# Performance work log

Measured on AMD Instinct MI355X. Metric: run time of the kernel, lower is better.

Reference implementation:

```python
import jax, jax.numpy as jnp
import numpy as np

HEADS = 8
DIM = 64      # dim
DH = 64       # dim_head
DK = 24       # dim_k (== dim_head_k * heads, required by reshape in forward)
DHK = 3       # dim_head_k (also conv groups)


def setup_inputs() -> dict:
    key = jax.random.key(0)
    ks = jax.random.split(key, 10)
    b, h, w = 4, 128, 128
    return {
        "x_in": jax.random.normal(ks[0], (b, h, w, DIM), jnp.float32),
        "illu_fea_trans": jax.random.normal(ks[1], (b, h, w, DIM), jnp.float32),
        "illu_map_trans": jax.random.normal(ks[2], (b, h, w, DK), jnp.float32),
        # Linear weights stored as [in, out] (torch stores [out, in]; math y = x @ W_in_out)
        "Wq": jax.random.normal(ks[3], (DIM, HEADS * DH), jnp.float32) * 0.05,
        "Wk": jax.random.normal(ks[4], (DK, HEADS * DHK), jnp.float32) * 0.05,
        "Wv": jax.random.normal(ks[5], (DIM, HEADS * DH), jnp.float32) * 0.05,
        "rescale": jnp.ones((HEADS, 1, 1), jnp.float32),
        "Wp": jax.random.normal(ks[6], (HEADS * DHK, DK), jnp.float32) * 0.05,
        "bp": jax.random.normal(ks[7], (DK,), jnp.float32) * 0.05,
        # grouped conv weights, OIHW: [out=24, in/groups=8, 3, 3]
        "conv1_w": jax.random.normal(ks[8], (DK, DK // DHK, 3, 3), jnp.float32) * 0.05,
        "conv2_w": jax.random.normal(ks[9], (DK, DK // DHK, 3, 3), jnp.float32) * 0.05,
    }


def _gconv(x_nchw, w_oihw):
    return jax.lax.conv_general_dilated(
        x_nchw, w_oihw, window_strides=(1, 1), padding='SAME',
        feature_group_count=DHK,
        dimension_numbers=('NCHW', 'OIHW', 'NCHW'))


def reference(x_in, illu_fea_trans, illu_map_trans, Wq, Wk, Wv, rescale, Wp, bp, conv1_w, conv2_w):
    b, h, w, c = x_in.shape
    n = h * w
    # projections
    q = (x_in.reshape(b, n, c) @ Wq).reshape(b, n, HEADS, DH)
    k_inp = illu_map_trans.reshape(b, n, DK) @ Wk            # [b, n, heads*dhk]
    v = (illu_fea_trans.reshape(b, n, c) @ Wv).reshape(b, n, HEADS, DH)
    kh = k_inp.reshape(b, n, HEADS, DHK)
    q = q / (DIM ** 0.5)  # note: scaled by sqrt(dim), not sqrt(dim_head)
    # channel-wise cross-attention: attn over channel dims, contracting tokens n
    attn = jnp.einsum('bnhk,bnhd->bhkd', kh, q) * rescale[None]  # [b, heads, dhk, dh]
    attn = jax.nn.softmax(attn, axis=-1)
    out = jnp.einsum('bhkd,bnhd->bnkh', attn, v)             # [b, n, dhk, heads]
    out = out.reshape(b, n, DHK * HEADS) @ Wp + bp           # proj
    out = out.reshape(b, h, w, DK)
    # positional branch: two grouped 3x3 convs with exact GELU on k_inp
    kx = k_inp.reshape(b, h, w, DK).transpose(0, 3, 1, 2)    # NCHW
    y = _gconv(kx, conv1_w)
    y = jax.nn.gelu(y, approximate=False)
    y = _gconv(y, conv2_w)
    return out + y.transpose(0, 2, 3, 1)
```

## Files before the change

### kernel.cpp

```cpp
#include <hip/hip_runtime.h>
#include <math.h>

#define HEADS 8
#define DIM   64
#define DK    24
#define DHK   3
#define BB    4
#define HH    128
#define WW    128
#define NN    (HH*WW)
#define QSCALE 0.125f

__global__ __launch_bounds__(256) void s_reduce(
    const float* __restrict__ imap,
    const float* __restrict__ x,
    float* __restrict__ Sp_part)
{
    __shared__ __align__(16) float smem[6160];
    float* xs   = smem;
    float* ms   = smem + 4096;
    float* part = smem;

    const int tid = threadIdx.x;
    const int blk = blockIdx.x;
    const int b = blk >> 8, chunk = blk & 255;
    const int w = tid >> 6, lane = tid & 63;
    const int cq = lane & 15;
    const int ig = lane >> 4;

    const long tok0 = (long)b * NN + chunk * 64;

    {
        const float4* xg = (const float4*)(x + tok0 * 64);
        float4* xs4 = (float4*)xs;
        #pragma unroll
        for (int e = 0; e < 4; ++e) xs4[tid + e * 256] = xg[tid + e * 256];
        const float4* mg = (const float4*)(imap + tok0 * 24);
        float4* ms4 = (float4*)ms;
        if (tid < 128) {
            ms4[tid]       = mg[tid];
            ms4[tid + 128] = mg[tid + 128];
            ms4[tid + 256] = mg[tid + 256];
        }
    }
    __syncthreads();

    float acc[6][4];
    #pragma unroll
    for (int r = 0; r < 6; ++r)
        #pragma unroll
        for (int q = 0; q < 4; ++q) acc[r][q] = 0.f;

    {
        const float* xp = xs + w * 16 * 64 + cq * 4;
        const float* mp = ms + w * 16 * 24 + ig * 6;
        #pragma unroll 4
        for (int t = 0; t < 16; ++t) {
            float4 xv = *(const float4*)(xp + t * 64);
            float2 m0 = *(const float2*)(mp + t * 24);
            float2 m1 = *(const float2*)(mp + t * 24 + 2);
            float2 m2 = *(const float2*)(mp + t * 24 + 4);
            float mm[6] = {m0.x, m0.y, m1.x, m1.y, m2.x, m2.y};
            #pragma unroll
            for (int r = 0; r < 6; ++r) {
                acc[r][0] += mm[r] * xv.x;
                acc[r][1] += mm[r] * xv.y;
                acc[r][2] += mm[r] * xv.z;
                acc[r][3] += mm[r] * xv.w;
            }
        }
    }
    __syncthreads();

    float* pp = part + w * 1540;
    #pragma unroll
    for (int r = 0; r < 6; ++r) {
        float4 v = {acc[r][0], acc[r][1], acc[r][2], acc[r][3]};
        *(float4*)(pp + (ig * 6 + r) * 64 + cq * 4) = v;
    }
    __syncthreads();

    for (int e = tid; e < 1536; e += 256) {
        Sp_part[(long)blk * 1536 + e] =
            part[e] + part[1540 + e] + part[3080 + e] + part[4620 + e];
    }
}

__global__ __launch_bounds__(256) void slab_reduce(
    const float* __restrict__ Sp_part,
    float* __restrict__ Sp)
{
    __shared__ float red[256];
    const int tid = threadIdx.x;
    const int blk = blockIdx.x;
    const int b = blk / 24, eg = blk % 24;
    const int w = tid >> 6, lane = tid & 63;
    const int e = eg * 64 + lane;

    const float* p = Sp_part + ((long)(b * 256 + w * 64)) * 1536 + e;
    float s = 0.f;
    #pragma unroll 16
    for (int sb = 0; sb < 64; ++sb) s += p[(long)sb * 1536];
    red[w * 64 + lane] = s;
    __syncthreads();

    if (tid < 64)
        Sp[b * 1536 + eg * 64 + tid] =
            red[tid] + red[64 + tid] + red[128 + tid] + red[192 + tid];
}

__global__ __launch_bounds__(1024) void attn_fused(
    const float* __restrict__ Sp,
    const float* __restrict__ Wk,
    const float* __restrict__ Wq,
    const float* __restrict__ Wv,
    const float* __restrict__ rescale,
    const float* __restrict__ Wp,
    float* __restrict__ Pt)
{
    __shared__ float Sp_l[1536];
    __shared__ float S_l[1536];
    __shared__ float att[1536];

    const int tid = threadIdx.x, b = blockIdx.x;
    const int w = tid >> 6, lane = tid & 63;

    for (int e = tid; e < 1536; e += 1024) Sp_l[e] = Sp[b * 1536 + e];
    __syncthreads();

    for (int e = tid; e < 1536; e += 1024) {
        const int c = e & 63, ch = e >> 6;
        float s = 0.f;
        #pragma unroll
        for (int i = 0; i < 24; ++i) s += Wk[i * 24 + ch] * Sp_l[i * 64 + c];
        S_l[e] = s;
    }
    __syncthreads();

    for (int e = tid; e < 1536; e += 1024) {
        const int d = e & 63, ch = e >> 6, h = ch / 3;
        const float* wq = Wq + h * 64 + d;
        const float* sr = S_l + ch * 64;
        float s = 0.f;
        #pragma unroll 8
        for (int c = 0; c < 64; ++c) s += sr[c] * wq[c * 512];
        att[e] = s * QSCALE * rescale[h];
    }
    __syncthreads();

    #pragma unroll
    for (int pass = 0; pass < 2; ++pass) {
        const int r = w + pass * 16;
        if (r < 24 && (pass == 0 || w < 8)) {
            float a = att[r * 64 + lane];
            float mx = a;
            #pragma unroll
            for (int off = 32; off >= 1; off >>= 1)
                mx = fmaxf(mx, __shfl_xor(mx, off, 64));
            float e = expf(a - mx);
            float sum = e;
            #pragma unroll
            for (int off = 32; off >= 1; off >>= 1)
                sum += __shfl_xor(sum, off, 64);
            att[r * 64 + lane] = e / sum;
        }
    }
    __syncthreads();

    for (int e = tid; e < 1536; e += 1024) {
        const int c = e & 63, ch = e >> 6, h = ch / 3;
        const float* pr = att + ch * 64;
        const float* wv = Wv + c * 512 + h * 64;
        float s = 0.f;
        #pragma unroll
        for (int d = 0; d < 64; ++d) s += pr[d] * wv[d];
        S_l[e] = s;
    }
    __syncthreads();

    for (int e = tid; e < 1536; e += 1024) {
        const int c = e & 63, o = e >> 6;
        float s = 0.f;
        #pragma unroll
        for (int k = 0; k < 3; ++k)
            #pragma unroll
            for (int h = 0; h < 8; ++h)
                s += S_l[(h * 3 + k) * 64 + c] * Wp[(k * 8 + h) * 24 + o];
        Pt[b * 1536 + e] = s;
    }
}

__global__ __launch_bounds__(192, 2) void conv_fused(
    const float* __restrict__ imap, const float* __restrict__ Wk,
    const float* __restrict__ c1w,  const float* __restrict__ fea,
    const float* __restrict__ c2w,  const float* __restrict__ Pt,
    const float* __restrict__ bp,   float* __restrict__ outp)
{
    __shared__ __align__(16) float smem[7152];
    float* kbuf = smem;
    float* feat = smem;
    float* y1l  = smem + 4352;

    const int tid = threadIdx.x;
    const int blk = blockIdx.x;
    const int b = blk >> 8, ti = (blk >> 4) & 15, tj = blk & 15;
    const int i0 = ti * 8, j0 = tj * 8;
    const int o = tid % 24, jj = tid / 24;
    const int g = o >> 3;

    if (tid < 144) {
        const int pi = tid / 12, pj = tid % 12;
        const int gi = i0 + pi - 2, gj = j0 + pj - 2;
        float kv[24];
        #pragma unroll
        for (int j = 0; j < 24; ++j) kv[j] = 0.f;
        if (gi >= 0 && gi < HH && gj >= 0 && gj < WW) {
            const float4* m4 = (const float4*)(imap + (((long)b * HH + gi) * WW + gj) * 24);
            float m[24];
            #pragma unroll
            for (int i = 0; i < 6; ++i) {
                float4 v = m4[i];
                m[4*i+0]=v.x; m[4*i+1]=v.y; m[4*i+2]=v.z; m[4*i+3]=v.w;
            }
            for (int i = 0; i < 24; ++i) {
                float mi = m[i];
                #pragma unroll
                for (int j = 0; j < 24; ++j) kv[j] += mi * Wk[i * 24 + j];
            }
        }
        #pragma unroll
        for (int j = 0; j < 24; ++j) kbuf[tid * 28 + j] = kv[j];
    }
    __syncthreads();

    {
        float wr[8][9];
        {
            const float4* wp = (const float4*)(c1w + o * 72);
            #pragma unroll
            for (int t = 0; t < 18; ++t) ((float4*)wr)[t] = wp[t];
        }
        for (int task = tid; task < 240; task += 192) {
            const int r = task / 24;
            float wc[3][3][8];
            #pragma unroll
            for (int slot = 0; slot < 2; ++slot)
                #pragma unroll
                for (int di = 0; di < 3; ++di) {
                    const float* p = kbuf + ((r + di) * 12 + slot) * 28 + g * 8;
                    *(float4*)&wc[slot][di][0] = *(const float4*)(p);
                    *(float4*)&wc[slot][di][4] = *(const float4*)(p + 4);
                }
            #pragma unroll
            for (int c = 0; c < 10; ++c) {
                const int s2 = (c + 2) % 3;
                #pragma unroll
                for (int di = 0; di < 3; ++di) {
                    const float* p = kbuf + ((r + di) * 12 + (c + 2)) * 28 + g * 8;
                    *(float4*)&wc[s2][di][0] = *(const float4*)(p);
                    *(float4*)&wc[s2][di][4] = *(const float4*)(p + 4);
                }
                float s = 0.f;
                #pragma unroll
                for (int dj = 0; dj < 3; ++dj) {
                    const int sl = (c + dj) % 3;
                    #pragma unroll
                    for (int di = 0; di < 3; ++di)
                        #pragma unroll
                        for (int ic = 0; ic < 8; ++ic)
                            s += wc[sl][di][ic] * wr[ic][di * 3 + dj];
                }
                const int gi = i0 + r - 1, gj = j0 + c - 1;
                float val = 0.f;
                if (gi >= 0 && gi < HH && gj >= 0 && gj < WW)
                    val = 0.5f * s * (1.f + erff(s * 0.70710678f));
                y1l[(r * 10 + c) * 28 + o] = val;
            }
        }
    }
    __syncthreads();

    {
        const float4* feaT4 = (const float4*)(fea + (((long)(b * HH + i0)) * WW + j0) * 64);
        float4* feat4 = (float4*)feat;
        for (int e = tid; e < 1024; e += 192) {
            const int pix = e >> 4, cq = e & 15;
            feat4[pix * 17 + cq] =
                feaT4[((long)(pix >> 3) * WW + (pix & 7)) * 16 + cq];
        }
    }
    __syncthreads();

    float wr[8][9];
    {
        const float4* wp = (const float4*)(c2w + o * 72);
        #pragma unroll
        for (int t = 0; t < 18; ++t) ((float4*)wr)[t] = wp[t];
    }

    float acc[8];
    {
        const float bo = bp[o];
        #pragma unroll
        for (int ii = 0; ii < 8; ++ii) acc[ii] = bo;
        const float4* pr4 = (const float4*)(Pt + b * 1536 + o * 64);
        for (int cq = 0; cq < 16; ++cq) {
            float4 p = pr4[cq];
            #pragma unroll
            for (int ii = 0; ii < 8; ++ii) {
                float4 f = ((const float4*)(feat + (ii * 8 + jj) * 68))[cq];
                acc[ii] += f.x * p.x + f.y * p.y + f.z * p.z + f.w * p.w;
            }
        }
    }

    float win[3][3][8];
    #define LROW(R, SLOT)                                                     \
    {                                                                         \
        const float* rp_ = y1l + ((R) * 10 + jj) * 28 + g * 8;                \
        *(float4*)&win[SLOT][0][0] = *(const float4*)(rp_);                   \
        *(float4*)&win[SLOT][0][4] = *(const float4*)(rp_ + 4);               \
        *(float4*)&win[SLOT][1][0] = *(const float4*)(rp_ + 28);              \
        *(float4*)&win[SLOT][1][4] = *(const float4*)(rp_ + 32);              \
        *(float4*)&win[SLOT][2][0] = *(const float4*)(rp_ + 56);              \
        *(float4*)&win[SLOT][2][4] = *(const float4*)(rp_ + 60);              \
    }

    LROW(0, 0)
    LROW(1, 1)
    #pragma unroll
    for (int ii = 0; ii < 8; ++ii) {
        LROW(ii + 2, (ii + 2) % 3)
        float s = 0.f;
        #pragma unroll
        for (int di = 0; di < 3; ++di) {
            const int slot = (ii + di) % 3;
            #pragma unroll
            for (int dj = 0; dj < 3; ++dj)
                #pragma unroll
                for (int ic = 0; ic < 8; ++ic)
                    s += win[slot][dj][ic] * wr[ic][di * 3 + dj];
        }
        outp[((long)((b * HH + i0 + ii) * WW + j0)) * 24 + tid] = acc[ii] + s;
    }
    #undef LROW
}

extern "C" void kernel_launch(void* const* d_in, const int* in_sizes, int n_in,
                              void* d_out, int out_size, void* d_ws, size_t ws_size,
                              hipStream_t stream) {
    const float* x_in    = (const float*)d_in[0];
    const float* fea     = (const float*)d_in[1];
    const float* imap    = (const float*)d_in[2];
    const float* Wq      = (const float*)d_in[3];
    const float* Wk      = (const float*)d_in[4];
    const float* Wv      = (const float*)d_in[5];
    const float* rescale = (const float*)d_in[6];
    const float* Wp      = (const float*)d_in[7];
    const float* bp      = (const float*)d_in[8];
    const float* c1w     = (const float*)d_in[9];
    const float* c2w     = (const float*)d_in[10];
    float* out = (float*)d_out;

    float* ws      = (float*)d_ws;
    float* Sp_part = ws;
    float* Sp      = ws + 1572864;
    float* Pt      = ws + 1579008;

    s_reduce<<<1024, 256, 0, stream>>>(imap, x_in, Sp_part);
    slab_reduce<<<96, 256, 0, stream>>>(Sp_part, Sp);
    attn_fused<<<4, 1024, 0, stream>>>(Sp, Wk, Wq, Wv, rescale, Wp, Pt);
    conv_fused<<<BB * 256, 192, 0, stream>>>(imap, Wk, c1w, fea, c2w, Pt, bp, out);
}
```

Before: 166.4 us.

## Fold attention projections into reduction kernels and drop the single-block attention kernel

Removes the attn_fused kernel, which ran on only 4 blocks. The Wk and Wq projections move into each s_reduce block, using linearity to project the per-chunk partial sums before the global reduction. The second reduction kernel now also does the softmax and Wv product per row. The Wp projection is recomputed per tile inside conv_fused. This removes one launch and a serialized low-parallelism stage, at the cost of redundant Wq and Wp matmuls in every block, plus extra shared memory and global reads of weights.

```diff
diff --git a/kernel.cpp b/kernel.cpp
--- a/kernel.cpp
+++ b/kernel.cpp
@@ -11,15 +11,21 @@
 #define NN    (HH*WW)
 #define QSCALE 0.125f
 
-__global__ __launch_bounds__(256) void s_reduce(
+__global__ __launch_bounds__(256) void s_reduce_proj(
     const float* __restrict__ imap,
     const float* __restrict__ x,
-    float* __restrict__ Sp_part)
+    const float* __restrict__ Wk,
+    const float* __restrict__ Wq,
+    const float* __restrict__ rescale,
+    float* __restrict__ att_part)
 {
-    __shared__ __align__(16) float smem[6160];
+    __shared__ __align__(16) float smem[7696];
     float* xs   = smem;
     float* ms   = smem + 4096;
     float* part = smem;
+    float* Sp_l = smem + 6160;
+    float* S_l  = smem;
+    float* wq_l = smem + 1536;
 
     const int tid = threadIdx.x;
     const int blk = blockIdx.x;
@@ -50,7 +56,6 @@
     for (int r = 0; r < 6; ++r)
         #pragma unroll
         for (int q = 0; q < 4; ++q) acc[r][q] = 0.f;
-
     {
         const float* xp = xs + w * 16 * 64 + cq * 4;
         const float* mp = ms + w * 16 * 24 + ig * 6;
@@ -80,126 +85,115 @@
     }
     __syncthreads();
 
+    for (int e = tid; e < 1536; e += 256)
+        Sp_l[e] = part[e] + part[1540 + e] + part[3080 + e] + part[4620 + e];
+    __syncthreads();
+
     for (int e = tid; e < 1536; e += 256) {
-        Sp_part[(long)blk * 1536 + e] =
-            part[e] + part[1540 + e] + part[3080 + e] + part[4620 + e];
+        const int c = e & 63, ch = e >> 6;
+        float s = 0.f;
+        #pragma unroll
+        for (int i = 0; i < 24; ++i) s += Wk[i * 24 + ch] * Sp_l[i * 64 + c];
+        S_l[e] = s;
+    }
+    __syncthreads();
+
+    const long outbase = (long)blk * 1536;
+    for (int h = 0; h < 8; ++h) {
+        {
+            float4* wq4 = (float4*)(smem + 1536);
+            const float4* Wq4 = (const float4*)Wq;
+            for (int t = tid; t < 1024; t += 256) {
+                const int c = t >> 4, r = t & 15;
+                wq4[c * 17 + r] = Wq4[c * 128 + h * 16 + r];
+            }
+        }
+        __syncthreads();
+        if (tid < 192) {
+            const int d = tid & 63, ch3 = tid >> 6;
+            const float* sr = S_l + (h * 3 + ch3) * 64;
+            float s = 0.f;
+            #pragma unroll 8
+            for (int c = 0; c < 64; ++c) s += sr[c] * wq_l[c * 68 + d];
+            att_part[outbase + h * 192 + tid] = s * QSCALE * rescale[h];
+        }
+        __syncthreads();
     }
 }
 
-__global__ __launch_bounds__(256) void slab_reduce(
-    const float* __restrict__ Sp_part,
-    float* __restrict__ Sp)
+__global__ __launch_bounds__(256) void row_attn(
+    const float* __restrict__ att_part,
+    const float* __restrict__ Wv,
+    float* __restrict__ Ms)
 {
     __shared__ float red[256];
-    const int tid = threadIdx.x;
-    const int blk = blockIdx.x;
-    const int b = blk / 24, eg = blk % 24;
-    const int w = tid >> 6, lane = tid & 63;
-    const int e = eg * 64 + lane;
-
-    const float* p = Sp_part + ((long)(b * 256 + w * 64)) * 1536 + e;
-    float s = 0.f;
-    #pragma unroll 16
-    for (int sb = 0; sb < 64; ++sb) s += p[(long)sb * 1536];
-    red[w * 64 + lane] = s;
-    __syncthreads();
-
+    __shared__ float pl[64];
+    __shared__ __align__(16) float wv_l[64 * 68];
+
+    const int tid = threadIdx.x, blk = blockIdx.x;
+    const int b = blk / 24, ch = blk % 24, h = ch / 3;
+    const int d = tid & 63, q = tid >> 6;
+
+    {
+        const float* p = att_part + ((long)(b * 256 + q * 64)) * 1536 + ch * 64 + d;
+        float s = 0.f;
+        #pragma unroll 16
+        for (int sb = 0; sb < 64; ++sb) s += p[(long)sb * 1536];
+        red[tid] = s;
+    }
+    __syncthreads();
+
+    if (tid < 64) {
+        float a = red[tid] + red[64 + tid] + red[128 + tid] + red[192 + tid];
+        float mx = a;
+        #pragma unroll
+        for (int off = 32; off >= 1; off >>= 1)
+            mx = fmaxf(mx, __shfl_xor(mx, off, 64));
+        float e = expf(a - mx);
+        float sum = e;
+        #pragma unroll
+        for (int off = 32; off >= 1; off >>= 1)
+            sum += __shfl_xor(sum, off, 64);
+        pl[tid] = e / sum;
+    }
+    {
+        float4* wv4 = (float4*)wv_l;
+        const float4* Wv4 = (const float4*)Wv;
+        for (int t = tid; t < 1024; t += 256) {
+            const int c = t >> 4, r = t & 15;
+            wv4[c * 17 + r] = Wv4[c * 128 + h * 16 + r];
+        }
+    }
+    __syncthreads();
+
+    {
+        const int c = tid & 63;
+        const float* wvr = wv_l + c * 68 + q * 16;
+        const float* pr = pl + q * 16;
+        float m = 0.f;
+        #pragma unroll
+        for (int j = 0; j < 16; ++j) m += pr[j] * wvr[j];
+        red[tid] = m;
+    }
+    __syncthreads();
     if (tid < 64)
-        Sp[b * 1536 + eg * 64 + tid] =
+        Ms[b * 1536 + ch * 64 + tid] =
             red[tid] + red[64 + tid] + red[128 + tid] + red[192 + tid];
-}
-
-__global__ __launch_bounds__(1024) void attn_fused(
-    const float* __restrict__ Sp,
-    const float* __restrict__ Wk,
-    const float* __restrict__ Wq,
-    const float* __restrict__ Wv,
-    const float* __restrict__ rescale,
-    const float* __restrict__ Wp,
-    float* __restrict__ Pt)
-{
-    __shared__ float Sp_l[1536];
-    __shared__ float S_l[1536];
-    __shared__ float att[1536];
-
-    const int tid = threadIdx.x, b = blockIdx.x;
-    const int w = tid >> 6, lane = tid & 63;
-
-    for (int e = tid; e < 1536; e += 1024) Sp_l[e] = Sp[b * 1536 + e];
-    __syncthreads();
-
-    for (int e = tid; e < 1536; e += 1024) {
-        const int c = e & 63, ch = e >> 6;
-        float s = 0.f;
-        #pragma unroll
-        for (int i = 0; i < 24; ++i) s += Wk[i * 24 + ch] * Sp_l[i * 64 + c];
-        S_l[e] = s;
-    }
-    __syncthreads();
-
-    for (int e = tid; e < 1536; e += 1024) {
-        const int d = e & 63, ch = e >> 6, h = ch / 3;
-        const float* wq = Wq + h * 64 + d;
-        const float* sr = S_l + ch * 64;
-        float s = 0.f;
-        #pragma unroll 8
-        for (int c = 0; c < 64; ++c) s += sr[c] * wq[c * 512];
-        att[e] = s * QSCALE * rescale[h];
-    }
-    __syncthreads();
-
-    #pragma unroll
-    for (int pass = 0; pass < 2; ++pass) {
-        const int r = w + pass * 16;
-        if (r < 24 && (pass == 0 || w < 8)) {
-            float a = att[r * 64 + lane];
-            float mx = a;
-            #pragma unroll
-            for (int off = 32; off >= 1; off >>= 1)
-                mx = fmaxf(mx, __shfl_xor(mx, off, 64));
-            float e = expf(a - mx);
-            float sum = e;
-            #pragma unroll
-            for (int off = 32; off >= 1; off >>= 1)
-                sum += __shfl_xor(sum, off, 64);
-            att[r * 64 + lane] = e / sum;
-        }
-    }
-    __syncthreads();
-
-    for (int e = tid; e < 1536; e += 1024) {
-        const int c = e & 63, ch = e >> 6, h = ch / 3;
-        const float* pr = att + ch * 64;
-        const float* wv = Wv + c * 512 + h * 64;
-        float s = 0.f;
-        #pragma unroll
-        for (int d = 0; d < 64; ++d) s += pr[d] * wv[d];
-        S_l[e] = s;
-    }
-    __syncthreads();
-
-    for (int e = tid; e < 1536; e += 1024) {
-        const int c = e & 63, o = e >> 6;
-        float s = 0.f;
-        #pragma unroll
-        for (int k = 0; k < 3; ++k)
-            #pragma unroll
-            for (int h = 0; h < 8; ++h)
-                s += S_l[(h * 3 + k) * 64 + c] * Wp[(k * 8 + h) * 24 + o];
-        Pt[b * 1536 + e] = s;
-    }
 }
 
 __global__ __launch_bounds__(192, 2) void conv_fused(
     const float* __restrict__ imap, const float* __restrict__ Wk,
     const float* __restrict__ c1w,  const float* __restrict__ fea,
-    const float* __restrict__ c2w,  const float* __restrict__ Pt,
-    const float* __restrict__ bp,   float* __restrict__ outp)
+    const float* __restrict__ c2w,  const float* __restrict__ Ms,
+    const float* __restrict__ Wp,   const float* __restrict__ bp,
+    float* __restrict__ outp)
 {
-    __shared__ __align__(16) float smem[7152];
+    __shared__ __align__(16) float smem[8784];
+    float* Ml   = smem;
     float* kbuf = smem;
     float* feat = smem;
     float* y1l  = smem + 4352;
+    float* ptl  = smem + 7152;
 
     const int tid = threadIdx.x;
     const int blk = blockIdx.x;
@@ -207,6 +201,22 @@
     const int i0 = ti * 8, j0 = tj * 8;
     const int o = tid % 24, jj = tid / 24;
     const int g = o >> 3;
+
+    {
+        for (int e = tid; e < 1536; e += 192) Ml[e] = Ms[b * 1536 + e];
+        __syncthreads();
+        for (int e = tid; e < 1536; e += 192) {
+            const int oo = e >> 6, c = e & 63;
+            float s = 0.f;
+            #pragma unroll
+            for (int k = 0; k < 3; ++k)
+                #pragma unroll
+                for (int h = 0; h < 8; ++h)
+                    s += Ml[(h * 3 + k) * 64 + c] * Wp[(k * 8 + h) * 24 + oo];
+            ptl[oo * 68 + c] = s;
+        }
+        __syncthreads();
+    }
 
     if (tid < 144) {
         const int pi = tid / 12, pj = tid % 12;
@@ -303,7 +313,7 @@
         const float bo = bp[o];
         #pragma unroll
         for (int ii = 0; ii < 8; ++ii) acc[ii] = bo;
-        const float4* pr4 = (const float4*)(Pt + b * 1536 + o * 64);
+        const float4* pr4 = (const float4*)(ptl + o * 68);
         for (int cq = 0; cq < 16; ++cq) {
             float4 p = pr4[cq];
             #pragma unroll
@@ -362,13 +372,11 @@
     const float* c2w     = (const float*)d_in[10];
     float* out = (float*)d_out;
 
-    float* ws      = (float*)d_ws;
-    float* Sp_part = ws;
-    float* Sp      = ws + 1572864;
-    float* Pt      = ws + 1579008;
-
-    s_reduce<<<1024, 256, 0, stream>>>(imap, x_in, Sp_part);
-    slab_reduce<<<96, 256, 0, stream>>>(Sp_part, Sp);
-    attn_fused<<<4, 1024, 0, stream>>>(Sp, Wk, Wq, Wv, rescale, Wp, Pt);
-    conv_fused<<<BB * 256, 192, 0, stream>>>(imap, Wk, c1w, fea, c2w, Pt, bp, out);
+    float* ws       = (float*)d_ws;
+    float* att_part = ws;
+    float* Ms       = ws + 1572864;
+
+    s_reduce_proj<<<1024, 256, 0, stream>>>(imap, x_in, Wk, Wq, rescale, att_part);
+    row_attn<<<96, 256, 0, stream>>>(att_part, Wv, Ms);
+    conv_fused<<<BB * 256, 192, 0, stream>>>(imap, Wk, c1w, fea, c2w, Ms, Wp, bp, out);
 }
```

New measurement: 166.4 us. No clear change (+0.0%).
